# Optimization experiments

Measured on AMD Instinct MI355X. Metric: run time of the kernel, lower is better.

Reference implementation:

```python
import jax, jax.numpy as jnp
import numpy as np

B, S, D, H = 2, 2048, 2048, 16
HD = D // H  # 128
THETA = 10000.0


def _rope_cos_sin(seq_len, head_dim):
    # matches LlamaRotaryEmbedding: inv_freq = 1/theta^(2i/d), emb = cat(freqs, freqs)
    inv_freq = 1.0 / (THETA ** (jnp.arange(0, head_dim, 2, dtype=jnp.float32) / head_dim))
    t = jnp.arange(seq_len, dtype=jnp.float32)
    freqs = jnp.einsum('s,d->sd', t, inv_freq)          # [S, HD/2]
    emb = jnp.concatenate([freqs, freqs], axis=-1)       # [S, HD]
    return jnp.cos(emb), jnp.sin(emb)


def _rotate_half(x):
    x1, x2 = jnp.split(x, 2, axis=-1)
    return jnp.concatenate([-x2, x1], axis=-1)


def setup_inputs() -> dict:
    key = jax.random.key(0)
    ks = jax.random.split(key, 5)
    scale = D ** -0.5
    x = jax.random.normal(ks[0], (B, S, D), jnp.float32)
    wq = jax.random.normal(ks[1], (D, D), jnp.float32) * scale
    wk = jax.random.normal(ks[2], (D, D), jnp.float32) * scale
    wv = jax.random.normal(ks[3], (D, D), jnp.float32) * scale
    wo = jax.random.normal(ks[4], (D, D), jnp.float32) * scale
    # additive causal mask (0 on/below diagonal, large negative above)
    causal = jnp.tril(jnp.ones((S, S), dtype=bool))
    mask = jnp.where(causal, 0.0, -1e9).astype(jnp.float32)[None, None]  # [1,1,S,S]
    return {"x": x, "wq": wq, "wk": wk, "wv": wv, "wo": wo, "mask": mask}


def reference(x, wq, wk, wv, wo, mask):
    b, s, d = x.shape
    # projections + head split: [b, H, s, HD]
    q = (x @ wq).reshape(b, s, H, HD).transpose(0, 2, 1, 3)
    k = (x @ wk).reshape(b, s, H, HD).transpose(0, 2, 1, 3)
    v = (x @ wv).reshape(b, s, H, HD).transpose(0, 2, 1, 3)
    # inline RoPE on q and k (positions 0..s-1 along the seq axis)
    cos, sin = _rope_cos_sin(s, HD)
    cos = cos[None, None]  # [1,1,s,HD]
    sin = sin[None, None]
    q = q * cos + _rotate_half(q) * sin
    k = k * cos + _rotate_half(k) * sin
    # eager attention: QK^T * scale + mask -> softmax -> @ V
    attn = jnp.einsum('bhqd,bhkd->bhqk', q, k) * (HD ** -0.5)
    attn = jax.nn.softmax(attn + mask, axis=-1)
    out = jnp.einsum('bhqk,bhkd->bhqd', attn, v)
    out = out.transpose(0, 2, 1, 3).reshape(b, s, d)
    return out @ wo
```

## Files before the change

### kernel.cpp

```cpp
#include <hip/hip_runtime.h>

#define S_LEN 2048
#define D_DIM 2048
#define NH 16
#define HD 128
#define NB 2
#define NROW (NB * S_LEN)
#define QKV_STR 6144

typedef unsigned short bf16;
typedef __attribute__((ext_vector_type(8))) short bf16x8;
typedef __attribute__((ext_vector_type(4))) float f32x4;
typedef __attribute__((ext_vector_type(16))) float f32x16;
typedef __attribute__((address_space(3))) unsigned int as3u;
typedef __attribute__((address_space(1))) unsigned int as1u;

__device__ __forceinline__ void gload16(const void* g, void* l) {
  __builtin_amdgcn_global_load_lds((const as1u*)g, (as3u*)l, 16, 0, 0);
}

__device__ __forceinline__ unsigned short f2bf(float f) {
  unsigned u = __builtin_bit_cast(unsigned, f);
  u += 0x7FFFu + ((u >> 16) & 1u);
  return (unsigned short)(u >> 16);
}
__device__ __forceinline__ float bf2f(unsigned short b) {
  return __builtin_bit_cast(float, (unsigned)b << 16);
}
__device__ __forceinline__ unsigned cvtpk(float lo, float hi) {
  unsigned r;
  asm("v_cvt_pk_bf16_f32 %0, %1, %2" : "=v"(r) : "v"(lo), "v"(hi));
  return r;
}
__device__ __forceinline__ float exp2a(float x) {
  float r;
  asm("v_exp_f32 %0, %1" : "=v"(r) : "v"(x));
  return r;
}


__global__ void rope_table_k(float2* __restrict__ tab) {
  int i = blockIdx.x * 256 + threadIdx.x;
  int s = i >> 6, d = i & 63;
  float invf = powf(10000.0f, -(float)d * (1.0f / 64.0f));
  float ang = (float)s * invf;
  tab[i] = make_float2(cosf(ang), sinf(ang));
}

__global__ void convert_x_k(const float* __restrict__ src, bf16* __restrict__ dst) {
  int i = (blockIdx.x * 256 + threadIdx.x) * 4;
  float4 v = *(const float4*)(src + i);
  ushort4 w;
  w.x = f2bf(v.x); w.y = f2bf(v.y); w.z = f2bf(v.z); w.w = f2bf(v.w);
  *(ushort4*)(dst + i) = w;
}

__global__ void transpose_w_k(const float* __restrict__ w0, const float* __restrict__ w1,
                              const float* __restrict__ w2, const float* __restrict__ w3,
                              bf16* __restrict__ wTall, bf16* __restrict__ wTo) {
  __shared__ float t[64][65];
  int z = blockIdx.z;
  const float* W = (z == 0) ? w0 : (z == 1) ? w1 : (z == 2) ? w2 : w3;
  bf16* Wt = (z == 3) ? wTo : wTall + (size_t)z * 2048 * D_DIM;
  int c0 = blockIdx.x * 64, r0 = blockIdx.y * 64;
  int tx = threadIdx.x & 63, ty = threadIdx.x >> 6;
#pragma unroll
  for (int i = 0; i < 16; ++i)
    t[ty + i * 4][tx] = W[(size_t)(r0 + ty + i * 4) * D_DIM + c0 + tx];
  __syncthreads();
#pragma unroll
  for (int i = 0; i < 16; ++i)
    Wt[(size_t)(c0 + ty + i * 4) * D_DIM + r0 + tx] = f2bf(t[tx][ty + i * 4]);
}


__device__ __forceinline__ void storec(bf16* p, float v) { *p = f2bf(v); }
__device__ __forceinline__ void storec(float* p, float v) { *p = v; }

template <typename OutT>
__global__ __launch_bounds__(256) void gemm_bt_k(
    const bf16* __restrict__ A, const bf16* __restrict__ Bt,
    OutT* __restrict__ C, int M, int N, int K) {
  __shared__ bf16 As[128 * 64];
  __shared__ bf16 Bs[128 * 64];
  const int tid = threadIdx.x;
  const int lane = tid & 63;
  const int wid = tid >> 6;
  const int bm = blockIdx.y * 128;
  const int bn = blockIdx.x * 128;
  const int wr = (wid >> 1) * 64;
  const int wc = (wid & 1) * 64;
  const int lr = lane & 15;
  const int kg = lane >> 4;

  f32x4 acc[4][4] = {};

  const int srow = lane >> 3;
  const int scol = ((lane & 7) ^ srow) * 8;
  const bf16* Ap = A + (size_t)(bm + wid * 32 + srow) * K + scol;
  const bf16* Bp = Bt + (size_t)(bn + wid * 32 + srow) * K + scol;
  bf16* Asd = &As[wid * 32 * 64];
  bf16* Bsd = &Bs[wid * 32 * 64];

  const int rx = (lr & 7) << 4;

  for (int k0 = 0; k0 < K; k0 += 64) {
    __syncthreads();
#pragma unroll
    for (int p = 0; p < 4; ++p) {
      gload16(Ap + (size_t)(p * 8) * K + k0, Asd + p * 8 * 64);
      gload16(Bp + (size_t)(p * 8) * K + k0, Bsd + p * 8 * 64);
    }
    __syncthreads();
    bf16x8 a[4][2], b[4][2];
#pragma unroll
    for (int m = 0; m < 4; ++m) {
      const char* rowp = (const char*)&As[(wr + m * 16 + lr) * 64];
#pragma unroll
      for (int kk = 0; kk < 2; ++kk)
        a[m][kk] = *(const bf16x8*)(rowp + ((kk * 64 + kg * 16) ^ rx));
    }
#pragma unroll
    for (int n = 0; n < 4; ++n) {
      const char* rowp = (const char*)&Bs[(wc + n * 16 + lr) * 64];
#pragma unroll
      for (int kk = 0; kk < 2; ++kk)
        b[n][kk] = *(const bf16x8*)(rowp + ((kk * 64 + kg * 16) ^ rx));
    }
#pragma unroll
    for (int kk = 0; kk < 2; ++kk)
#pragma unroll
      for (int m = 0; m < 4; ++m)
#pragma unroll
        for (int n = 0; n < 4; ++n)
          acc[m][n] = __builtin_amdgcn_mfma_f32_16x16x32_bf16(a[m][kk], b[n][kk], acc[m][n], 0, 0, 0);
  }

#pragma unroll
  for (int m = 0; m < 4; ++m) {
    int row0 = bm + wr + m * 16 + kg * 4;
#pragma unroll
    for (int n = 0; n < 4; ++n) {
      int col = bn + wc + n * 16 + lr;
#pragma unroll
      for (int r = 0; r < 4; ++r)
        storec(&C[(size_t)(row0 + r) * N + col], acc[m][n][r]);
    }
  }
}

__global__ __launch_bounds__(256) void gemm_qkv_k(
    const bf16* __restrict__ A, const bf16* __restrict__ Bt,
    bf16* __restrict__ QKV, bf16* __restrict__ Vt,
    const float2* __restrict__ tab) {
  const int K = 2048;
  __shared__ bf16 As[128 * 64];
  __shared__ bf16 Bs[128 * 64];
  const int tid = threadIdx.x;
  const int lane = tid & 63;
  const int wid = tid >> 6;
  const int bm = blockIdx.y * 128;
  const int bn = blockIdx.x * 128;
  const int wr = (wid >> 1) * 64;
  const int wc2 = (wid & 1) * 32;
  const int lr = lane & 15;
  const int kg = lane >> 4;

  f32x4 acc[4][4] = {};

  const int srow = lane >> 3;
  const int scol = ((lane & 7) ^ srow) * 8;
  const bf16* Ap = A + (size_t)(bm + wid * 32 + srow) * K + scol;
  const bf16* Bp = Bt + (size_t)(bn + wid * 32 + srow) * K + scol;
  bf16* Asd = &As[wid * 32 * 64];
  bf16* Bsd = &Bs[wid * 32 * 64];

  const int rx = (lr & 7) << 4;

  for (int k0 = 0; k0 < K; k0 += 64) {
    __syncthreads();
#pragma unroll
    for (int p = 0; p < 4; ++p) {
      gload16(Ap + (size_t)(p * 8) * K + k0, Asd + p * 8 * 64);
      gload16(Bp + (size_t)(p * 8) * K + k0, Bsd + p * 8 * 64);
    }
    __syncthreads();
    bf16x8 a[4][2], b[4][2];
#pragma unroll
    for (int m = 0; m < 4; ++m) {
      const char* rowp = (const char*)&As[(wr + m * 16 + lr) * 64];
#pragma unroll
      for (int kk = 0; kk < 2; ++kk)
        a[m][kk] = *(const bf16x8*)(rowp + ((kk * 64 + kg * 16) ^ rx));
    }
#pragma unroll
    for (int n = 0; n < 4; ++n) {
      int bcol = wc2 + (n & 1) * 16 + (n >> 1) * 64;
      const char* rowp = (const char*)&Bs[(bcol + lr) * 64];
#pragma unroll
      for (int kk = 0; kk < 2; ++kk)
        b[n][kk] = *(const bf16x8*)(rowp + ((kk * 64 + kg * 16) ^ rx));
    }
#pragma unroll
    for (int kk = 0; kk < 2; ++kk)
#pragma unroll
      for (int m = 0; m < 4; ++m)
#pragma unroll
        for (int n = 0; n < 4; ++n)
          acc[m][n] = __builtin_amdgcn_mfma_f32_16x16x32_bf16(a[m][kk], b[n][kk], acc[m][n], 0, 0, 0);
  }

  if (bn < 4096) {
    const float sc = (bn < 2048) ? 0.12751743f : 1.0f;
#pragma unroll
    for (int m = 0; m < 4; ++m) {
      int row0 = bm + wr + m * 16 + kg * 4;
#pragma unroll
      for (int j = 0; j < 2; ++j) {
        int d = wc2 + j * 16 + lr;
#pragma unroll
        for (int r = 0; r < 4; ++r) {
          int s_pos = (row0 + r) & (S_LEN - 1);
          float2 cs = tab[s_pos * 64 + d];
          float x1 = acc[m][j][r], x2 = acc[m][j + 2][r];
          bf16* rowp = QKV + (size_t)(row0 + r) * QKV_STR + bn + d;
          rowp[0]  = f2bf((x1 * cs.x - x2 * cs.y) * sc);
          rowp[64] = f2bf((x2 * cs.x + x1 * cs.y) * sc);
        }
      }
    }
  } else {
    int b = bm >> 11;
    int h = (bn - 4096) >> 7;
    bf16* vt = Vt + (size_t)(b * 16 + h) * HD * S_LEN;
#pragma unroll
    for (int m = 0; m < 4; ++m) {
      int s = (bm + wr + m * 16 + kg * 4) & (S_LEN - 1);
#pragma unroll
      for (int n = 0; n < 4; ++n) {
        int d = wc2 + (n & 1) * 16 + (n >> 1) * 64 + lr;
        ushort4 pk;
        pk.x = f2bf(acc[m][n][0]); pk.y = f2bf(acc[m][n][1]);
        pk.z = f2bf(acc[m][n][2]); pk.w = f2bf(acc[m][n][3]);
        *(ushort4*)(vt + (size_t)d * S_LEN + s) = pk;
      }
    }
  }
}

#define FBODY(T, CUR0, CUR1, NXT0, NXT1)                                         \
  {                                                                              \
    const int kv0_ = (T) * 64;                                                   \
    stageV(kv0_ + 64, ((T) + 1) & 1);                                            \
    stageK(kv0_ + 192, kb_st);                                                   \
    kb_st = (kb_st == 2) ? 0 : kb_st + 1;                                        \
    if (kv0_ + 64 <= qw0 + 31) {                                                 \
      NXT0 = 0.0f; NXT1 = 0.0f;                                                  \
      const bf16* krow0_ = &sh[kb_rd * 8192] + (size_t)l31 * 128;                \
      const bf16* krow1_ = krow0_ + 32 * 128;                                    \
      _Pragma("unroll")                                                          \
      for (int ks = 0; ks < 8; ++ks) {                                           \
        int cb_ = ((ks * 32) ^ kxor) >> 1;                                       \
        bf16x8 kf0_ = *(const bf16x8*)(krow0_ + cb_);                            \
        bf16x8 kf1_ = *(const bf16x8*)(krow1_ + cb_);                            \
        NXT0 = __builtin_amdgcn_mfma_f32_32x32x16_bf16(kf0_, qf[ks], NXT0, 0, 0, 0); \
        NXT1 = __builtin_amdgcn_mfma_f32_32x32x16_bf16(kf1_, qf[ks], NXT1, 0, 0, 0); \
      }                                                                          \
    }                                                                            \
    kb_rd = (kb_rd == 2) ? 0 : kb_rd + 1;                                        \
    if (kv0_ <= qw0 + 31) {                                                      \
      if (kv0_ + 63 > qw0) {                                                     \
        _Pragma("unroll")                                                        \
        for (int r = 0; r < 16; ++r) {                                           \
          int kvg_ = kv0_ + (r & 3) + 8 * (r >> 2) + 4 * h;                      \
          if (kvg_ > q) CUR0[r] = -3.0e38f;                                      \
          if (kvg_ + 32 > q) CUR1[r] = -3.0e38f;                                 \
        }                                                                        \
      }                                                                          \
      float tm_[8];                                                              \
      _Pragma("unroll")                                                          \
      for (int r = 0; r < 8; ++r)                                                \
        tm_[r] = fmaxf(fmaxf(CUR0[r], CUR0[r + 8]), fmaxf(CUR1[r], CUR1[r + 8])); \
      _Pragma("unroll")                                                          \
      for (int r = 0; r < 4; ++r) tm_[r] = fmaxf(tm_[r], tm_[r + 4]);            \
      float mt_ = fmaxf(fmaxf(tm_[0], tm_[1]), fmaxf(tm_[2], tm_[3]));           \
      mt_ = fmaxf(mt_, __shfl_xor(mt_, 32));                                     \
      if (__any(mt_ > m_run + 8.0f)) {                                           \
        float mnew_ = fmaxf(m_run, mt_);                                         \
        float alpha_ = exp2a(m_run - mnew_);                                     \
        l_run *= alpha_;                                                         \
        _Pragma("unroll")                                                        \
        for (int n = 0; n < 4; ++n)                                              \
          _Pragma("unroll")                                                      \
          for (int r = 0; r < 16; ++r) ot[n][r] *= alpha_;                       \
        m_run = mnew_;                                                           \
      }                                                                          \
      float rs_[16];                                                             \
      _Pragma("unroll")                                                          \
      for (int r = 0; r < 16; ++r) {                                             \
        CUR0[r] = exp2a(CUR0[r] - m_run);                                        \
        CUR1[r] = exp2a(CUR1[r] - m_run);                                        \
        rs_[r] = CUR0[r] + CUR1[r];                                              \
      }                                                                          \
      _Pragma("unroll")                                                          \
      for (int r = 0; r < 8; ++r) rs_[r] += rs_[r + 8];                          \
      _Pragma("unroll")                                                          \
      for (int r = 0; r < 4; ++r) rs_[r] += rs_[r + 4];                          \
      float rsum_ = (rs_[0] + rs_[1]) + (rs_[2] + rs_[3]);                       \
      rsum_ += __shfl_xor(rsum_, 32);                                            \
      l_run += rsum_;                                                            \
      unsigned wd0_[8], wd1_[8];                                                 \
      _Pragma("unroll")                                                          \
      for (int j = 0; j < 8; ++j) {                                              \
        wd0_[j] = cvtpk(CUR0[2 * j], CUR0[2 * j + 1]);                           \
        wd1_[j] = cvtpk(CUR1[2 * j], CUR1[2 * j + 1]);                           \
      }                                                                          \
      const bf16* Vbuf_ = &sh[24576 + ((T) & 1) * 8192];                         \
      _Pragma("unroll")                                                          \
      for (int t4 = 0; t4 < 4; ++t4) {                                           \
        const unsigned* wdp_ = (t4 >> 1) ? wd1_ : wd0_;                          \
        int a0_ = 4 * (t4 & 1) + 2 * h;                                          \
        int sidx_ = 4 * (t4 & 1) + 2 * (1 - h);                                  \
        unsigned s0_ = (unsigned)__shfl_xor((int)wdp_[sidx_], 32);               \
        unsigned s1_ = (unsigned)__shfl_xor((int)wdp_[sidx_ + 1], 32);           \
        unsigned pb4_[4];                                                        \
        pb4_[0] = h ? s0_ : wdp_[a0_];                                           \
        pb4_[1] = h ? s1_ : wdp_[a0_ + 1];                                       \
        pb4_[2] = h ? wdp_[a0_] : s0_;                                           \
        pb4_[3] = h ? wdp_[a0_ + 1] : s1_;                                       \
        bf16x8 pb_ = __builtin_bit_cast(bf16x8, *(uint4*)pb4_);                  \
        int cb_ = ((t4 * 32) ^ vxor) >> 1;                                       \
        _Pragma("unroll")                                                        \
        for (int n = 0; n < 4; ++n) {                                            \
          bf16x8 va_ = *(const bf16x8*)(Vbuf_ + (size_t)(32 * n + l31) * 64 + cb_); \
          ot[n] = __builtin_amdgcn_mfma_f32_32x32x16_bf16(va_, pb_, ot[n], 0, 0, 0); \
        }                                                                        \
      }                                                                          \
    }                                                                            \
    asm volatile("s_waitcnt vmcnt(4)" ::: "memory");                             \
    __builtin_amdgcn_sched_barrier(0);                                           \
    __builtin_amdgcn_s_barrier();                                                \
  }

__global__ __launch_bounds__(256, 2) void flash_attn_k(
    const bf16* __restrict__ Q, const bf16* __restrict__ Kb,
    const bf16* __restrict__ Vt, bf16* __restrict__ O) {
  __shared__ bf16 sh[40960];
  const int tid = threadIdx.x;
  const int lane = tid & 63;
  const int w = tid >> 6;
  const int h = lane >> 5;
  const int l31 = lane & 31;
  const int bh = blockIdx.y;
  const int b = bh >> 4;
  const int hh = bh & 15;
  const int xr = (bh & 16) ? blockIdx.x : (gridDim.x - 1 - blockIdx.x);
  const int qb = xr * 128;
  const int qw0 = qb + 32 * w;
  const int q = qw0 + l31;

  const bf16* qp = Q + (size_t)(b * S_LEN + q) * QKV_STR + hh * HD + h * 8;
  bf16x8 qf[8];
#pragma unroll
  for (int ks = 0; ks < 8; ++ks) qf[ks] = *(const bf16x8*)(qp + ks * 16);

  f32x16 ot[4] = {};
  float m_run = -3.0e38f, l_run = 0.f;

  const bf16* Kg = Kb + (size_t)(b * S_LEN) * QKV_STR + hh * HD;
  const bf16* Vg = Vt + (size_t)bh * HD * S_LEN;

  const int kst_row = 16 * w + (lane >> 4);
  const int vst_row = 32 * w + (lane >> 3);
  const int vst_col = (((lane & 7) ^ (lane >> 3)) << 3);
  const int kxor = (16 * h) ^ ((l31 & 15) << 4);
  const int vxor = (16 * h) ^ ((l31 & 7) << 4);

  auto stageK = [&](int kv0, int buf) {
#pragma unroll
    for (int jj = 0; jj < 4; ++jj) {
      int kr = (kv0 + kst_row + jj * 4) & (S_LEN - 1);
      gload16(Kg + (size_t)kr * QKV_STR + (((lane & 15) ^ (jj * 4 + (lane >> 4))) << 3),
              &sh[buf * 8192 + (16 * w + jj * 4) * 128]);
    }
  };
  auto stageV = [&](int kv0, int buf) {
    int c = (kv0 & (S_LEN - 1)) + vst_col;
#pragma unroll
    for (int jj = 0; jj < 4; ++jj) {
      int vr = vst_row + jj * 8;
      gload16(Vg + (size_t)vr * S_LEN + c, &sh[24576 + buf * 8192 + (32 * w + jj * 8) * 64]);
    }
  };

  stageK(0, 0);
  stageV(0, 0);
  stageK(64, 1);
  stageK(128, 2);
  asm volatile("s_waitcnt vmcnt(12)" ::: "memory");
  __builtin_amdgcn_sched_barrier(0);
  __builtin_amdgcn_s_barrier();

  f32x16 stA0 = 0.0f, stA1 = 0.0f, stB0, stB1;
  {
    const bf16* krow0 = &sh[0] + (size_t)l31 * 128;
    const bf16* krow1 = krow0 + 32 * 128;
#pragma unroll
    for (int ks = 0; ks < 8; ++ks) {
      int cb = ((ks * 32) ^ kxor) >> 1;
      bf16x8 kf0 = *(const bf16x8*)(krow0 + cb);
      bf16x8 kf1 = *(const bf16x8*)(krow1 + cb);
      stA0 = __builtin_amdgcn_mfma_f32_32x32x16_bf16(kf0, qf[ks], stA0, 0, 0, 0);
      stA1 = __builtin_amdgcn_mfma_f32_32x32x16_bf16(kf1, qf[ks], stA1, 0, 0, 0);
    }
  }
  asm volatile("s_waitcnt vmcnt(4)" ::: "memory");
  __builtin_amdgcn_sched_barrier(0);
  __builtin_amdgcn_s_barrier();

  int kb_st = 0;
  int kb_rd = 1;
  const int nt = qb / 64 + 2;
  int t = 0;
  for (; t + 1 < nt; t += 2) {
    FBODY(t, stA0, stA1, stB0, stB1);
    FBODY(t + 1, stB0, stB1, stA0, stA1);
  }
  if (t < nt) FBODY(t, stA0, stA1, stB0, stB1);

  asm volatile("s_waitcnt vmcnt(0)" ::: "memory");
  __builtin_amdgcn_s_barrier();

  float inv = 1.0f / l_run;
  bf16* ow = &sh[w * 4096];
#pragma unroll
  for (int n = 0; n < 4; ++n)
#pragma unroll
    for (int rq = 0; rq < 4; ++rq) {
      int dbase = 32 * n + 8 * rq + 4 * h;
      unsigned u0 = cvtpk(ot[n][4 * rq + 0] * inv, ot[n][4 * rq + 1] * inv);
      unsigned u1 = cvtpk(ot[n][4 * rq + 2] * inv, ot[n][4 * rq + 3] * inv);
      uint2 uu = make_uint2(u0, u1);
      *(uint2*)(ow + l31 * 128 + (dbase ^ ((l31 & 15) << 3))) = uu;
    }
  __syncthreads();
#pragma unroll
  for (int p = 0; p < 8; ++p) {
    int qr = p * 4 + (lane >> 4);
    int ce = ((((lane & 15) << 4) ^ ((qr & 15) << 4)) >> 1);
    bf16x8 vrow = *(const bf16x8*)(ow + qr * 128 + ce);
    *(bf16x8*)(O + (size_t)(b * S_LEN + qw0 + qr) * D_DIM + hh * HD + (lane & 15) * 8) = vrow;
  }
}


extern "C" void kernel_launch(void* const* d_in, const int* in_sizes, int n_in,
                              void* d_out, int out_size, void* d_ws, size_t ws_size,
                              hipStream_t stream) {
  (void)in_sizes; (void)n_in; (void)out_size; (void)ws_size;
  const float* x  = (const float*)d_in[0];
  const float* wq = (const float*)d_in[1];
  const float* wk = (const float*)d_in[2];
  const float* wv = (const float*)d_in[3];
  const float* wo = (const float*)d_in[4];
  float* out = (float*)d_out;

  char* ws = (char*)d_ws;
  const size_t MB = 1u << 20;
  bf16* xb    = (bf16*)(ws + 0 * MB);
  bf16* Ob    = xb;
  bf16* wTall = (bf16*)(ws + 16 * MB);
  bf16* wTo   = (bf16*)(ws + 40 * MB);
  bf16* QKV   = (bf16*)(ws + 48 * MB);
  bf16* Vtb   = (bf16*)(ws + 96 * MB);
  float2* tab = (float2*)(ws + 112 * MB);

  rope_table_k<<<512, 256, 0, stream>>>(tab);
  convert_x_k<<<8192, 256, 0, stream>>>(x, xb);
  transpose_w_k<<<dim3(32, 32, 4), 256, 0, stream>>>(wq, wk, wv, wo, wTall, wTo);

  gemm_qkv_k<<<dim3(QKV_STR / 128, NROW / 128), 256, 0, stream>>>(
      xb, wTall, QKV, Vtb, tab);

  flash_attn_k<<<dim3(S_LEN / 128, NB * NH), 256, 0, stream>>>(
      QKV, QKV + 2048, Vtb, Ob);

  gemm_bt_k<float><<<dim3(D_DIM / 128, NROW / 128), 256, 0, stream>>>(
      Ob, wTo, out, NROW, D_DIM, D_DIM);
}
```

Baseline: 286.8 us.

## Stage QKV GEMM epilogue through LDS and raise wave priority around MFMA loops

The QKV projection epilogue now writes RoPE-rotated Q/K and transposed V tiles into swizzled shared memory first, then writes them to global memory as coalesced 16-byte row stores. This replaces scattered 2-byte and 8-byte strided stores, which matter most for the V transpose. The flash attention kernel also wraps its QK^T and PV MFMA loops in s_setprio(1)/s_setprio(0) so the wave issuing matrix math gets scheduling priority. The cost is extra barriers and a round trip through LDS in the epilogue.

```diff
diff --git a/kernel.cpp b/kernel.cpp
--- a/kernel.cpp
+++ b/kernel.cpp
@@ -154,8 +154,9 @@
     bf16* __restrict__ QKV, bf16* __restrict__ Vt,
     const float2* __restrict__ tab) {
   const int K = 2048;
-  __shared__ bf16 As[128 * 64];
-  __shared__ bf16 Bs[128 * 64];
+  __shared__ bf16 smem[16384];
+  bf16* As = smem;
+  bf16* Bs = smem + 8192;
   const int tid = threadIdx.x;
   const int lane = tid & 63;
   const int wid = tid >> 6;
@@ -210,40 +211,63 @@
           acc[m][n] = __builtin_amdgcn_mfma_f32_16x16x32_bf16(a[m][kk], b[n][kk], acc[m][n], 0, 0, 0);
   }
 
+  __syncthreads();
+  char* eb = (char*)smem;
+
   if (bn < 4096) {
     const float sc = (bn < 2048) ? 0.12751743f : 1.0f;
 #pragma unroll
     for (int m = 0; m < 4; ++m) {
-      int row0 = bm + wr + m * 16 + kg * 4;
+      int sl = wr + m * 16 + kg * 4;
 #pragma unroll
       for (int j = 0; j < 2; ++j) {
         int d = wc2 + j * 16 + lr;
 #pragma unroll
         for (int r = 0; r < 4; ++r) {
-          int s_pos = (row0 + r) & (S_LEN - 1);
+          int row = sl + r;
+          int s_pos = (bm + row) & (S_LEN - 1);
           float2 cs = tab[s_pos * 64 + d];
           float x1 = acc[m][j][r], x2 = acc[m][j + 2][r];
-          bf16* rowp = QKV + (size_t)(row0 + r) * QKV_STR + bn + d;
-          rowp[0]  = f2bf((x1 * cs.x - x2 * cs.y) * sc);
-          rowp[64] = f2bf((x2 * cs.x + x1 * cs.y) * sc);
+          char* base = eb + row * 256;
+          *(bf16*)(base + ((d * 2) ^ ((row & 7) << 4)))        = f2bf((x1 * cs.x - x2 * cs.y) * sc);
+          *(bf16*)(base + (((d + 64) * 2) ^ ((row & 7) << 4))) = f2bf((x2 * cs.x + x1 * cs.y) * sc);
         }
       }
     }
+    __syncthreads();
+    int row = tid >> 1, ch = (tid & 1) * 64;
+    bf16* dst = QKV + (size_t)(bm + row) * QKV_STR + bn + ch;
+    char* src = eb + row * 256;
+#pragma unroll
+    for (int i = 0; i < 8; ++i) {
+      int c = ch + i * 8;
+      *(bf16x8*)(dst + i * 8) = *(const bf16x8*)(src + ((c * 2) ^ ((row & 7) << 4)));
+    }
   } else {
-    int b = bm >> 11;
-    int h = (bn - 4096) >> 7;
-    bf16* vt = Vt + (size_t)(b * 16 + h) * HD * S_LEN;
 #pragma unroll
     for (int m = 0; m < 4; ++m) {
-      int s = (bm + wr + m * 16 + kg * 4) & (S_LEN - 1);
+      int sl = wr + m * 16 + kg * 4;
 #pragma unroll
       for (int n = 0; n < 4; ++n) {
         int d = wc2 + (n & 1) * 16 + (n >> 1) * 64 + lr;
         ushort4 pk;
         pk.x = f2bf(acc[m][n][0]); pk.y = f2bf(acc[m][n][1]);
         pk.z = f2bf(acc[m][n][2]); pk.w = f2bf(acc[m][n][3]);
-        *(ushort4*)(vt + (size_t)d * S_LEN + s) = pk;
+        *(ushort4*)(eb + d * 256 + ((sl * 2) ^ ((d & 7) << 4))) = pk;
       }
+    }
+    __syncthreads();
+    int b = bm >> 11;
+    int h = (bn - 4096) >> 7;
+    bf16* vt = Vt + (size_t)(b * 16 + h) * HD * S_LEN;
+    int d = tid >> 1, sh2 = (tid & 1) * 64;
+    int sbase = bm & (S_LEN - 1);
+    char* src = eb + d * 256;
+#pragma unroll
+    for (int i = 0; i < 8; ++i) {
+      int s = sh2 + i * 8;
+      *(bf16x8*)(vt + (size_t)d * S_LEN + sbase + s) =
+          *(const bf16x8*)(src + ((s * 2) ^ ((d & 7) << 4)));
     }
   }
 }
@@ -258,6 +282,7 @@
       NXT0 = 0.0f; NXT1 = 0.0f;                                                  \
       const bf16* krow0_ = &sh[kb_rd * 8192] + (size_t)l31 * 128;                \
       const bf16* krow1_ = krow0_ + 32 * 128;                                    \
+      __builtin_amdgcn_s_setprio(1);                                             \
       _Pragma("unroll")                                                          \
       for (int ks = 0; ks < 8; ++ks) {                                           \
         int cb_ = ((ks * 32) ^ kxor) >> 1;                                       \
@@ -266,6 +291,7 @@
         NXT0 = __builtin_amdgcn_mfma_f32_32x32x16_bf16(kf0_, qf[ks], NXT0, 0, 0, 0); \
         NXT1 = __builtin_amdgcn_mfma_f32_32x32x16_bf16(kf1_, qf[ks], NXT1, 0, 0, 0); \
       }                                                                          \
+      __builtin_amdgcn_s_setprio(0);                                             \
     }                                                                            \
     kb_rd = (kb_rd == 2) ? 0 : kb_rd + 1;                                        \
     if (kv0_ <= qw0 + 31) {                                                      \
@@ -316,6 +342,7 @@
         wd1_[j] = cvtpk(CUR1[2 * j], CUR1[2 * j + 1]);                           \
       }                                                                          \
       const bf16* Vbuf_ = &sh[24576 + ((T) & 1) * 8192];                         \
+      __builtin_amdgcn_s_setprio(1);                                             \
       _Pragma("unroll")                                                          \
       for (int t4 = 0; t4 < 4; ++t4) {                                           \
         const unsigned* wdp_ = (t4 >> 1) ? wd1_ : wd0_;                          \
@@ -336,6 +363,7 @@
           ot[n] = __builtin_amdgcn_mfma_f32_32x32x16_bf16(va_, pb_, ot[n], 0, 0, 0); \
         }                                                                        \
       }                                                                          \
+      __builtin_amdgcn_s_setprio(0);                                             \
     }                                                                            \
     asm volatile("s_waitcnt vmcnt(4)" ::: "memory");                             \
     __builtin_amdgcn_sched_barrier(0);                                           \
@@ -405,6 +433,7 @@
   {
     const bf16* krow0 = &sh[0] + (size_t)l31 * 128;
     const bf16* krow1 = krow0 + 32 * 128;
+    __builtin_amdgcn_s_setprio(1);
 #pragma unroll
     for (int ks = 0; ks < 8; ++ks) {
       int cb = ((ks * 32) ^ kxor) >> 1;
@@ -413,6 +442,7 @@
       stA0 = __builtin_amdgcn_mfma_f32_32x32x16_bf16(kf0, qf[ks], stA0, 0, 0, 0);
       stA1 = __builtin_amdgcn_mfma_f32_32x32x16_bf16(kf1, qf[ks], stA1, 0, 0, 0);
     }
+    __builtin_amdgcn_s_setprio(0);
   }
   asm volatile("s_waitcnt vmcnt(4)" ::: "memory");
   __builtin_amdgcn_sched_barrier(0);
```

Result: no change. 289.7 us (+1.0%).
